# Optimization experiments

Measured on AMD Instinct MI355X. Metric: run time of the kernel, lower is better.

## Reference

```python
import jax, jax.numpy as jnp
import numpy as np
import math

D_MODEL = 1024
NUM_HEADS = 16
D_K = D_MODEL // NUM_HEADS
B, S = 2, 2048


def _linear_weight(key, out_f, in_f):
    return jax.random.normal(key, (out_f, in_f), jnp.float32) * math.sqrt(2.0 / in_f)


def setup_inputs() -> dict:
    key = jax.random.key(0)
    ks = jax.random.split(key, 5)
    x = jax.random.normal(ks[0], (B, S, D_MODEL), jnp.float32)
    return {
        "x": x,
        "Wq": _linear_weight(ks[1], D_MODEL, D_MODEL),
        "bq": jnp.zeros((D_MODEL,), jnp.float32),
        "Wk": _linear_weight(ks[2], D_MODEL, D_MODEL),
        "bk": jnp.zeros((D_MODEL,), jnp.float32),
        "Wv": _linear_weight(ks[3], D_MODEL, D_MODEL),
        "bv": jnp.zeros((D_MODEL,), jnp.float32),
        "Wo": _linear_weight(ks[4], D_MODEL, D_MODEL),
        "bo": jnp.zeros((D_MODEL,), jnp.float32),
    }


def reference(x, Wq, bq, Wk, bk, Wv, bv, Wo, bo):
    b, s, _ = x.shape
    # Projections: x @ W.T + b (CustomLinear stores weight as (out, in))
    q = jnp.einsum("bsd,ed->bse", x, Wq) + bq
    k = jnp.einsum("bsd,ed->bse", x, Wk) + bk
    v = jnp.einsum("bsd,ed->bse", x, Wv) + bv
    # (b, h, s, d_k)
    q = q.reshape(b, s, NUM_HEADS, D_K).transpose(0, 2, 1, 3)
    k = k.reshape(b, s, NUM_HEADS, D_K).transpose(0, 2, 1, 3)
    v = v.reshape(b, s, NUM_HEADS, D_K).transpose(0, 2, 1, 3)
    # Scaled dot-product attention with fully materialized scores (faithful)
    scores = jnp.einsum("bhqd,bhkd->bhqk", q, k) / math.sqrt(D_K)
    attn = jax.nn.softmax(scores, axis=-1)
    out = jnp.einsum("bhqk,bhkd->bhqd", attn, v)
    out = out.transpose(0, 2, 1, 3).reshape(b, s, D_MODEL)
    return jnp.einsum("bsd,ed->bse", out, Wo) + bo
```

## Files before the change

kernel.cpp:

```cpp
#include <hip/hip_runtime.h>
#include <hip/hip_bf16.h>

using bf16 = __hip_bfloat16;
typedef __attribute__((ext_vector_type(8))) short short8;
typedef __attribute__((ext_vector_type(4))) short s4v;
typedef __attribute__((ext_vector_type(4))) float float4v;
typedef __attribute__((ext_vector_type(4))) float f32x4;

#define MFMA16(a, b, c) __builtin_amdgcn_mfma_f32_16x16x32_bf16((a), (b), (c), 0, 0, 0)

#define GLD_LDS16(g, l)                                            \
    __builtin_amdgcn_global_load_lds(                              \
        (const __attribute__((address_space(1))) void*)(g),        \
        (__attribute__((address_space(3))) void*)(l), 16, 0, 0)

constexpr int Bc = 2;
constexpr int Sc = 2048;
constexpr int Hc = 16;
constexpr int DKc = 64;
constexpr int Dc = 1024;
constexpr size_t MEG = 1024 * 1024;

union BFU { bf16 h; short s; };

__device__ inline short bfbits(float f) {
    BFU u; u.h = __float2bfloat16(f); return u.s;
}

__device__ inline short8 load_cvt8(const float* __restrict__ p) {
    f32x4 a = *(const f32x4*)p;
    f32x4 b = *(const f32x4*)(p + 4);
    short8 r;
    r[0] = bfbits(a[0]); r[1] = bfbits(a[1]); r[2] = bfbits(a[2]); r[3] = bfbits(a[3]);
    r[4] = bfbits(b[0]); r[5] = bfbits(b[1]); r[6] = bfbits(b[2]); r[7] = bfbits(b[3]);
    return r;
}

__global__ __launch_bounds__(256) void cvt_kernel(
    const float* __restrict__ x, const float* __restrict__ Wq,
    const float* __restrict__ Wk, const float* __restrict__ Wv,
    const float* __restrict__ Wo, bf16* __restrict__ dst)
{
    const size_t i = ((size_t)blockIdx.x * 256 + threadIdx.x) * 8;
    const float* s;
    if      (i < 4 * MEG) s = x  + i;
    else if (i < 5 * MEG) s = Wq + (i - 4 * MEG);
    else if (i < 6 * MEG) s = Wk + (i - 5 * MEG);
    else if (i < 7 * MEG) s = Wv + (i - 6 * MEG);
    else                  s = Wo + (i - 7 * MEG);
    *(short8*)(dst + i) = load_cvt8(s);
}

__global__ __launch_bounds__(256) void qkv_gemm_kernel(
    const bf16* __restrict__ x,
    const bf16* __restrict__ Wq, const float* __restrict__ bq,
    const bf16* __restrict__ Wk, const float* __restrict__ bk,
    const bf16* __restrict__ Wv, const float* __restrict__ bv,
    bf16* __restrict__ q_ws, bf16* __restrict__ k_ws, bf16* __restrict__ v_ws)
{
    constexpr int BM = 128, BN = 128, BK = 32;
    __shared__ __align__(16) bf16 sA[BM * BK];
    __shared__ __align__(16) bf16 sB[BN * BK];

    const int bx = blockIdx.x;
    const int sel = bx >> 3;
    const int n0 = (bx & 7) * BN;
    const int m0 = blockIdx.y * BM;

    const bf16* __restrict__ Wsel = (sel == 0) ? Wq : ((sel == 1) ? Wk : Wv);
    const float* __restrict__ bsel = (sel == 0) ? bq : ((sel == 1) ? bk : bv);

    const int t = threadIdx.x;
    const int lane = t & 63;
    const int wave = t >> 6;
    const int ln = lane & 15;
    const int qd = lane >> 4;
    const int wm = (wave >> 1) * 64;
    const int wn = (wave & 1) * 64;

    const int gr = lane >> 2;
    const int gc = (lane & 3) * 8;

    float4v acc[4][4];
#pragma unroll
    for (int i = 0; i < 4; i++)
#pragma unroll
        for (int j = 0; j < 4; j++) acc[i][j] = (float4v)0.0f;

    for (int kk = 0; kk < Dc; kk += BK) {
        __syncthreads();
#pragma unroll
        for (int cc = 0; cc < 2; cc++) {
            const int c = wave * 2 + cc;
            GLD_LDS16(x    + (size_t)(m0 + c * 16 + gr) * Dc + kk + gc, &sA[c * 512]);
            GLD_LDS16(Wsel + (size_t)(n0 + c * 16 + gr) * Dc + kk + gc, &sB[c * 512]);
        }
        __syncthreads();

        short8 af[4], wf[4];
#pragma unroll
        for (int i = 0; i < 4; i++)
            af[i] = *(const short8*)&sA[(wm + i * 16 + ln) * BK + qd * 8];
#pragma unroll
        for (int j = 0; j < 4; j++)
            wf[j] = *(const short8*)&sB[(wn + j * 16 + ln) * BK + qd * 8];
#pragma unroll
        for (int i = 0; i < 4; i++)
#pragma unroll
            for (int j = 0; j < 4; j++)
                acc[i][j] = MFMA16(af[i], wf[j], acc[i][j]);
    }

    constexpr float QSCALE = 0.125f * 1.44269504088896f;

#pragma unroll
    for (int j = 0; j < 4; j++) {
        const int n = n0 + wn + j * 16 + ln;
        const float bias = bsel[n];
        const int h_ = n >> 6, d_ = n & 63;
#pragma unroll
        for (int i = 0; i < 4; i++) {
            const int mbase = m0 + wm + i * 16 + qd * 4;
            if (sel == 2) {
                const int b_ = mbase >> 11, s_ = mbase & 2047;
                s4v pk;
#pragma unroll
                for (int r = 0; r < 4; r++)
                    pk[r] = bfbits(acc[i][j][r] + bias);
                *(s4v*)&v_ws[(((size_t)(b_ * Hc + h_)) * DKc + d_) * Sc + s_] = pk;
            } else {
#pragma unroll
                for (int r = 0; r < 4; r++) {
                    const int m = mbase + r;
                    const int b_ = m >> 11, s_ = m & 2047;
                    float v = acc[i][j][r] + bias;
                    if (sel == 0) v *= QSCALE;
                    const bf16 o = __float2bfloat16(v);
                    if (sel == 0)
                        q_ws[(((size_t)(b_ * Hc + h_)) * Sc + s_) * DKc + d_] = o;
                    else
                        k_ws[(((size_t)(b_ * Hc + h_)) * Sc + s_) * DKc + d_] = o;
                }
            }
        }
    }
}

__global__ __launch_bounds__(512, 4) void attn_kernel(
    const bf16* __restrict__ q_ws, const bf16* __restrict__ k_ws,
    const bf16* __restrict__ v_ws, bf16* __restrict__ ao_ws)
{
    constexpr int LQP = 76;
    __shared__ __align__(16) bf16 sK[2][64 * 64];
    __shared__ __align__(16) bf16 sV[2][64 * 64];
    __shared__ __align__(16) short sP[8][16 * LQP];

    const int bh = blockIdx.x;
    const int qt = blockIdx.y;
    const int t = threadIdx.x;
    const int lane = t & 63;
    const int wave = t >> 6;
    const int ln = lane & 15;
    const int qd = lane >> 4;
    short* const sPw = sP[wave];

    const bf16* __restrict__ Qbase = q_ws + (size_t)bh * Sc * DKc + qt * 128 * DKc;
    const bf16* __restrict__ Kbase = k_ws + (size_t)bh * Sc * DKc;
    const bf16* __restrict__ Vbase = v_ws + (size_t)bh * DKc * Sc;

    const int rloc = lane >> 3;
    const int blk = lane & 7;

    short8 qf[2];
#pragma unroll
    for (int ks = 0; ks < 2; ks++)
        qf[ks] = *(const short8*)
            (Qbase + (size_t)(wave * 16 + ln) * DKc + ks * 32 + qd * 8);

    {
        const int row = wave * 8 + rloc;
        const int gb = blk ^ (row & 7);
        GLD_LDS16(Kbase + (size_t)row * DKc + gb * 8, &sK[0][wave * 512]);
        GLD_LDS16(Vbase + (size_t)row * Sc + gb * 8, &sV[0][wave * 512]);
    }

    short8 ones8;
    {
        const short ob = (ln == 0) ? (short)0x3F80 : (short)0;
#pragma unroll
        for (int i = 0; i < 8; i++) ones8[i] = ob;
    }

    float4v oacc[5];
#pragma unroll
    for (int j = 0; j < 5; j++) oacc[j] = (float4v)0.0f;

    for (int kt = 0; kt < Sc / 64; kt++) {
        const int cur = kt & 1;
        __syncthreads();
        if (kt + 1 < Sc / 64) {
            const int nxt = (kt + 1) & 1;
            const int row = wave * 8 + rloc;
            const int gb = blk ^ (row & 7);
            GLD_LDS16(Kbase + (size_t)((kt + 1) * 64 + row) * DKc + gb * 8,
                      &sK[nxt][wave * 512]);
            GLD_LDS16(Vbase + (size_t)row * Sc + (kt + 1) * 64 + gb * 8,
                      &sV[nxt][wave * 512]);
        }

        float4v sacc[4];
#pragma unroll
        for (int j = 0; j < 4; j++) sacc[j] = (float4v)0.0f;
        __builtin_amdgcn_s_setprio(1);
#pragma unroll
        for (int ks = 0; ks < 2; ks++) {
#pragma unroll
            for (int j = 0; j < 4; j++) {
                const int row = j * 16 + ln;
                const short8 ak = *(const short8*)
                    &sK[cur][row * 64 + (((ks * 4 + qd) ^ (row & 7)) << 3)];
                sacc[j] = MFMA16(ak, qf[ks], sacc[j]);
            }
        }
        __builtin_amdgcn_s_setprio(0);

#pragma unroll
        for (int j = 0; j < 4; j++) {
            s4v pk;
#pragma unroll
            for (int r = 0; r < 4; r++)
                pk[r] = bfbits(exp2f(sacc[j][r]));
            *(s4v*)&sPw[ln * LQP + j * 16 + qd * 4] = pk;
        }

        __builtin_amdgcn_s_setprio(1);
#pragma unroll
        for (int ks = 0; ks < 2; ks++) {
            const s4v p0 = *(const s4v*)&sPw[ln * LQP + ks * 32 + qd * 8];
            const s4v p1 = *(const s4v*)&sPw[ln * LQP + ks * 32 + qd * 8 + 4];
            const short8 ap = __builtin_shufflevector(p0, p1, 0, 1, 2, 3, 4, 5, 6, 7);
#pragma unroll
            for (int j = 0; j < 4; j++) {
                const int row = j * 16 + ln;
                const short8 bv_ = *(const short8*)
                    &sV[cur][row * 64 + (((ks * 4 + qd) ^ (row & 7)) << 3)];
                oacc[j] = MFMA16(ap, bv_, oacc[j]);
            }
            oacc[4] = MFMA16(ap, ones8, oacc[4]);
        }
        __builtin_amdgcn_s_setprio(0);
    }

    const int b_ = bh >> 4, h_ = bh & 15;
#pragma unroll
    for (int r = 0; r < 4; r++) {
        const float l = __shfl(oacc[4][r], lane & 48, 64);
        const float inv = 1.0f / l;
        const int s_ = qt * 128 + wave * 16 + qd * 4 + r;
#pragma unroll
        for (int j = 0; j < 4; j++) {
            const int d_ = j * 16 + ln;
            ao_ws[(((size_t)(b_ * Sc + s_)) * Hc + h_) * DKc + d_] =
                __float2bfloat16(oacc[j][r] * inv);
        }
    }
}

__global__ __launch_bounds__(256) void out_gemm_kernel(
    const bf16* __restrict__ A, const bf16* __restrict__ Wo,
    const float* __restrict__ bo, float* __restrict__ out)
{
    constexpr int BM = 128, BN = 128, BK = 32;
    __shared__ __align__(16) bf16 sA[BM * BK];
    __shared__ __align__(16) bf16 sB[BN * BK];

    const int n0 = blockIdx.x * BN;
    const int m0 = blockIdx.y * BM;

    const int t = threadIdx.x;
    const int lane = t & 63;
    const int wave = t >> 6;
    const int ln = lane & 15;
    const int qd = lane >> 4;
    const int wm = (wave >> 1) * 64;
    const int wn = (wave & 1) * 64;

    const int gr = lane >> 2;
    const int gc = (lane & 3) * 8;

    float4v acc[4][4];
#pragma unroll
    for (int i = 0; i < 4; i++)
#pragma unroll
        for (int j = 0; j < 4; j++) acc[i][j] = (float4v)0.0f;

    for (int kk = 0; kk < Dc; kk += BK) {
        __syncthreads();
#pragma unroll
        for (int cc = 0; cc < 2; cc++) {
            const int c = wave * 2 + cc;
            GLD_LDS16(A  + (size_t)(m0 + c * 16 + gr) * Dc + kk + gc, &sA[c * 512]);
            GLD_LDS16(Wo + (size_t)(n0 + c * 16 + gr) * Dc + kk + gc, &sB[c * 512]);
        }
        __syncthreads();

        short8 af[4], wf[4];
#pragma unroll
        for (int i = 0; i < 4; i++)
            af[i] = *(const short8*)&sA[(wm + i * 16 + ln) * BK + qd * 8];
#pragma unroll
        for (int j = 0; j < 4; j++)
            wf[j] = *(const short8*)&sB[(wn + j * 16 + ln) * BK + qd * 8];
#pragma unroll
        for (int i = 0; i < 4; i++)
#pragma unroll
            for (int j = 0; j < 4; j++)
                acc[i][j] = MFMA16(af[i], wf[j], acc[i][j]);
    }

#pragma unroll
    for (int j = 0; j < 4; j++) {
        const int n = n0 + wn + j * 16 + ln;
        const float bias = bo[n];
#pragma unroll
        for (int i = 0; i < 4; i++) {
            const int mbase = m0 + wm + i * 16 + qd * 4;
#pragma unroll
            for (int r = 0; r < 4; r++) {
                const int m = mbase + r;
                out[(size_t)m * Dc + n] = acc[i][j][r] + bias;
            }
        }
    }
}

extern "C" void kernel_launch(void* const* d_in, const int* in_sizes, int n_in,
                              void* d_out, int out_size, void* d_ws, size_t ws_size,
                              hipStream_t stream)
{
    const float* x  = (const float*)d_in[0];
    const float* Wq = (const float*)d_in[1];
    const float* bq = (const float*)d_in[2];
    const float* Wk = (const float*)d_in[3];
    const float* bk = (const float*)d_in[4];
    const float* Wv = (const float*)d_in[5];
    const float* bv = (const float*)d_in[6];
    const float* Wo = (const float*)d_in[7];
    const float* bo = (const float*)d_in[8];
    float* out = (float*)d_out;

    bf16* base  = (bf16*)d_ws;
    bf16* q_ws  = base;
    bf16* k_ws  = base + 4 * MEG;
    bf16* v_ws  = base + 8 * MEG;
    bf16* ao_ws = base + 12 * MEG;
    bf16* xb    = base + 16 * MEG;
    bf16* wqb   = base + 20 * MEG;
    bf16* wkb   = base + 21 * MEG;
    bf16* wvb   = base + 22 * MEG;
    bf16* wob   = base + 23 * MEG;

    cvt_kernel<<<dim3(4096), 256, 0, stream>>>(x, Wq, Wk, Wv, Wo, xb);
    qkv_gemm_kernel<<<dim3(24, 32), 256, 0, stream>>>(
        xb, wqb, bq, wkb, bk, wvb, bv, q_ws, k_ws, v_ws);
    attn_kernel<<<dim3(32, 16), 512, 0, stream>>>(q_ws, k_ws, v_ws, ao_ws);
    out_gemm_kernel<<<dim3(8, 32), 256, 0, stream>>>(ao_ws, wob, bo, out);
}
```

Measured before the change: 198.2 us.

## Split attention over two KV halves and merge with a combine kernel

```diff
diff --git a/kernel.cpp b/kernel.cpp
--- a/kernel.cpp
+++ b/kernel.cpp
@@ -25,6 +25,10 @@
 
 __device__ inline short bfbits(float f) {
     BFU u; u.h = __float2bfloat16(f); return u.s;
+}
+
+__device__ inline float bits2f(short s) {
+    BFU u; u.s = s; return __bfloat162float(u.h);
 }
 
 __device__ inline short8 load_cvt8(const float* __restrict__ p) {
@@ -146,17 +150,20 @@
     }
 }
 
-__global__ __launch_bounds__(512, 4) void attn_kernel(
+__global__ __launch_bounds__(512, 6) void attn_kernel(
     const bf16* __restrict__ q_ws, const bf16* __restrict__ k_ws,
-    const bf16* __restrict__ v_ws, bf16* __restrict__ ao_ws)
+    const bf16* __restrict__ v_ws, bf16* __restrict__ po0,
+    bf16* __restrict__ po1, float* __restrict__ l_ws)
 {
     constexpr int LQP = 76;
+    constexpr int NKT = 16;
     __shared__ __align__(16) bf16 sK[2][64 * 64];
     __shared__ __align__(16) bf16 sV[2][64 * 64];
     __shared__ __align__(16) short sP[8][16 * LQP];
 
     const int bh = blockIdx.x;
     const int qt = blockIdx.y;
+    const int sp = blockIdx.z;
     const int t = threadIdx.x;
     const int lane = t & 63;
     const int wave = t >> 6;
@@ -165,8 +172,8 @@
     short* const sPw = sP[wave];
 
     const bf16* __restrict__ Qbase = q_ws + (size_t)bh * Sc * DKc + qt * 128 * DKc;
-    const bf16* __restrict__ Kbase = k_ws + (size_t)bh * Sc * DKc;
-    const bf16* __restrict__ Vbase = v_ws + (size_t)bh * DKc * Sc;
+    const bf16* __restrict__ Kbase = k_ws + ((size_t)bh * Sc + sp * 1024) * DKc;
+    const bf16* __restrict__ Vbase = v_ws + (size_t)bh * DKc * Sc + sp * 1024;
 
     const int rloc = lane >> 3;
     const int blk = lane & 7;
@@ -195,10 +202,10 @@
 #pragma unroll
     for (int j = 0; j < 5; j++) oacc[j] = (float4v)0.0f;
 
-    for (int kt = 0; kt < Sc / 64; kt++) {
+    for (int kt = 0; kt < NKT; kt++) {
         const int cur = kt & 1;
         __syncthreads();
-        if (kt + 1 < Sc / 64) {
+        if (kt + 1 < NKT) {
             const int nxt = (kt + 1) & 1;
             const int row = wave * 8 + rloc;
             const int gb = blk ^ (row & 7);
@@ -252,6 +259,13 @@
     }
 
     const int b_ = bh >> 4, h_ = bh & 15;
+    bf16* __restrict__ po = sp ? po1 : po0;
+    if (ln == 0) {
+#pragma unroll
+        for (int r = 0; r < 4; r++)
+            l_ws[(size_t)(sp * 32 + bh) * Sc + qt * 128 + wave * 16 + qd * 4 + r] =
+                oacc[4][r];
+    }
 #pragma unroll
     for (int r = 0; r < 4; r++) {
         const float l = __shfl(oacc[4][r], lane & 48, 64);
@@ -260,10 +274,33 @@
 #pragma unroll
         for (int j = 0; j < 4; j++) {
             const int d_ = j * 16 + ln;
-            ao_ws[(((size_t)(b_ * Sc + s_)) * Hc + h_) * DKc + d_] =
+            po[(((size_t)(b_ * Sc + s_)) * Hc + h_) * DKc + d_] =
                 __float2bfloat16(oacc[j][r] * inv);
         }
     }
+}
+
+__global__ __launch_bounds__(256) void combine_kernel(
+    bf16* po0, const bf16* __restrict__ po1, const float* __restrict__ l_ws)
+{
+    const size_t gid = (size_t)blockIdx.x * 256 + threadIdx.x;
+    const size_t e = gid * 8;
+    const int flat = (int)(e >> 6);
+    const int h_ = flat & 15;
+    const int bs = flat >> 4;
+    const int b_ = bs >> 11, s_ = bs & 2047;
+    const int bh = b_ * Hc + h_;
+    const float l0 = l_ws[(size_t)bh * Sc + s_];
+    const float l1 = l_ws[(size_t)(32 + bh) * Sc + s_];
+    const float inv = 1.0f / (l0 + l1);
+    const float w0 = l0 * inv, w1 = l1 * inv;
+    const short8 a = *(const short8*)(po0 + e);
+    const short8 b = *(const short8*)(po1 + e);
+    short8 o;
+#pragma unroll
+    for (int i = 0; i < 8; i++)
+        o[i] = bfbits(bits2f(a[i]) * w0 + bits2f(b[i]) * w1);
+    *(short8*)(po0 + e) = o;
 }
 
 __global__ __launch_bounds__(256) void out_gemm_kernel(
@@ -355,7 +392,9 @@
     bf16* v_ws  = base + 8 * MEG;
     bf16* ao_ws = base + 12 * MEG;
     bf16* xb    = base + 16 * MEG;
+    bf16* po1   = xb;
     bf16* wqb   = base + 20 * MEG;
+    float* l_ws = (float*)wqb;
     bf16* wkb   = base + 21 * MEG;
     bf16* wvb   = base + 22 * MEG;
     bf16* wob   = base + 23 * MEG;
@@ -363,6 +402,8 @@
     cvt_kernel<<<dim3(4096), 256, 0, stream>>>(x, Wq, Wk, Wv, Wo, xb);
     qkv_gemm_kernel<<<dim3(24, 32), 256, 0, stream>>>(
         xb, wqb, bq, wkb, bk, wvb, bv, q_ws, k_ws, v_ws);
-    attn_kernel<<<dim3(32, 16), 512, 0, stream>>>(q_ws, k_ws, v_ws, ao_ws);
+    attn_kernel<<<dim3(32, 16, 2), 512, 0, stream>>>(
+        q_ws, k_ws, v_ws, ao_ws, po1, l_ws);
+    combine_kernel<<<dim3(2048), 256, 0, stream>>>(ao_ws, po1, l_ws);
     out_gemm_kernel<<<dim3(8, 32), 256, 0, stream>>>(ao_ws, wob, bo, out);
 }
```

Result: slower. 208.4 us (+5.1%).

## Double-buffer LDS tiles and XOR-swizzle layout in projection GEMMs

Applied to the files above, without the earlier changes.

```diff
diff --git a/kernel.cpp b/kernel.cpp
--- a/kernel.cpp
+++ b/kernel.cpp
@@ -58,9 +58,9 @@
     const bf16* __restrict__ Wv, const float* __restrict__ bv,
     bf16* __restrict__ q_ws, bf16* __restrict__ k_ws, bf16* __restrict__ v_ws)
 {
-    constexpr int BM = 128, BN = 128, BK = 32;
-    __shared__ __align__(16) bf16 sA[BM * BK];
-    __shared__ __align__(16) bf16 sB[BN * BK];
+    constexpr int BM = 128, BN = 128, BK = 32, NT = Dc / BK;
+    __shared__ __align__(16) bf16 sA[2][BM * BK];
+    __shared__ __align__(16) bf16 sB[2][BN * BK];
 
     const int bx = blockIdx.x;
     const int sel = bx >> 3;
@@ -78,8 +78,23 @@
     const int wm = (wave >> 1) * 64;
     const int wn = (wave & 1) * 64;
 
-    const int gr = lane >> 2;
-    const int gc = (lane & 3) * 8;
+    const int rloc = lane >> 2;
+    const int blk = lane & 3;
+    const int gb = (blk ^ ((rloc >> 1) & 3)) * 8;
+    const int xr = (qd ^ ((ln >> 1) & 3)) << 3;
+
+    auto stage = [&](int buf, int kk) {
+#pragma unroll
+        for (int cc = 0; cc < 4; cc++) {
+            const int cid = wave * 4 + cc;
+            if (cid < 8)
+                GLD_LDS16(x + (size_t)(m0 + cid * 16 + rloc) * Dc + kk + gb,
+                          &sA[buf][cid * 512]);
+            else
+                GLD_LDS16(Wsel + (size_t)(n0 + (cid - 8) * 16 + rloc) * Dc + kk + gb,
+                          &sB[buf][(cid - 8) * 512]);
+        }
+    };
 
     float4v acc[4][4];
 #pragma unroll
@@ -87,23 +102,19 @@
 #pragma unroll
         for (int j = 0; j < 4; j++) acc[i][j] = (float4v)0.0f;
 
-    for (int kk = 0; kk < Dc; kk += BK) {
+    stage(0, 0);
+    for (int tt = 0; tt < NT; tt++) {
+        const int cur = tt & 1;
         __syncthreads();
-#pragma unroll
-        for (int cc = 0; cc < 2; cc++) {
-            const int c = wave * 2 + cc;
-            GLD_LDS16(x    + (size_t)(m0 + c * 16 + gr) * Dc + kk + gc, &sA[c * 512]);
-            GLD_LDS16(Wsel + (size_t)(n0 + c * 16 + gr) * Dc + kk + gc, &sB[c * 512]);
-        }
-        __syncthreads();
+        if (tt + 1 < NT) stage(cur ^ 1, (tt + 1) * BK);
 
         short8 af[4], wf[4];
 #pragma unroll
         for (int i = 0; i < 4; i++)
-            af[i] = *(const short8*)&sA[(wm + i * 16 + ln) * BK + qd * 8];
+            af[i] = *(const short8*)&sA[cur][(wm + i * 16 + ln) * BK + xr];
 #pragma unroll
         for (int j = 0; j < 4; j++)
-            wf[j] = *(const short8*)&sB[(wn + j * 16 + ln) * BK + qd * 8];
+            wf[j] = *(const short8*)&sB[cur][(wn + j * 16 + ln) * BK + xr];
 #pragma unroll
         for (int i = 0; i < 4; i++)
 #pragma unroll
@@ -270,9 +281,9 @@
     const bf16* __restrict__ A, const bf16* __restrict__ Wo,
     const float* __restrict__ bo, float* __restrict__ out)
 {
-    constexpr int BM = 128, BN = 128, BK = 32;
-    __shared__ __align__(16) bf16 sA[BM * BK];
-    __shared__ __align__(16) bf16 sB[BN * BK];
+    constexpr int BM = 128, BN = 128, BK = 32, NT = Dc / BK;
+    __shared__ __align__(16) bf16 sA[2][BM * BK];
+    __shared__ __align__(16) bf16 sB[2][BN * BK];
 
     const int n0 = blockIdx.x * BN;
     const int m0 = blockIdx.y * BM;
@@ -285,8 +296,23 @@
     const int wm = (wave >> 1) * 64;
     const int wn = (wave & 1) * 64;
 
-    const int gr = lane >> 2;
-    const int gc = (lane & 3) * 8;
+    const int rloc = lane >> 2;
+    const int blk = lane & 3;
+    const int gb = (blk ^ ((rloc >> 1) & 3)) * 8;
+    const int xr = (qd ^ ((ln >> 1) & 3)) << 3;
+
+    auto stage = [&](int buf, int kk) {
+#pragma unroll
+        for (int cc = 0; cc < 4; cc++) {
+            const int cid = wave * 4 + cc;
+            if (cid < 8)
+                GLD_LDS16(A + (size_t)(m0 + cid * 16 + rloc) * Dc + kk + gb,
+                          &sA[buf][cid * 512]);
+            else
+                GLD_LDS16(Wo + (size_t)(n0 + (cid - 8) * 16 + rloc) * Dc + kk + gb,
+                          &sB[buf][(cid - 8) * 512]);
+        }
+    };
 
     float4v acc[4][4];
 #pragma unroll
@@ -294,23 +320,19 @@
 #pragma unroll
         for (int j = 0; j < 4; j++) acc[i][j] = (float4v)0.0f;
 
-    for (int kk = 0; kk < Dc; kk += BK) {
+    stage(0, 0);
+    for (int tt = 0; tt < NT; tt++) {
+        const int cur = tt & 1;
         __syncthreads();
-#pragma unroll
-        for (int cc = 0; cc < 2; cc++) {
-            const int c = wave * 2 + cc;
-            GLD_LDS16(A  + (size_t)(m0 + c * 16 + gr) * Dc + kk + gc, &sA[c * 512]);
-            GLD_LDS16(Wo + (size_t)(n0 + c * 16 + gr) * Dc + kk + gc, &sB[c * 512]);
-        }
-        __syncthreads();
+        if (tt + 1 < NT) stage(cur ^ 1, (tt + 1) * BK);
 
         short8 af[4], wf[4];
 #pragma unroll
         for (int i = 0; i < 4; i++)
-            af[i] = *(const short8*)&sA[(wm + i * 16 + ln) * BK + qd * 8];
+            af[i] = *(const short8*)&sA[cur][(wm + i * 16 + ln) * BK + xr];
 #pragma unroll
         for (int j = 0; j < 4; j++)
-            wf[j] = *(const short8*)&sB[(wn + j * 16 + ln) * BK + qd * 8];
+            wf[j] = *(const short8*)&sB[cur][(wn + j * 16 + ln) * BK + xr];
 #pragma unroll
         for (int i = 0; i < 4; i++)
 #pragma unroll
```

Result: no change. 197.0 us (-0.6%).
